# Optimization experiments

Hardware: AMD Instinct MI355X
Metric: run time of the kernel (lower is better)

Reference implementation:

```python
import jax, jax.numpy as jnp
import numpy as np

EPS = 1e-8  # torch F.cosine_similarity default eps


def setup_inputs() -> dict:
    key = jax.random.key(0)
    k1, k2 = jax.random.split(key)
    x = jax.random.normal(k1, (16384, 1024), dtype=jnp.float32)
    label = jax.random.randint(k2, (16384, 64), 0, 2).astype(jnp.int64)
    w = jnp.asarray(10.0, dtype=jnp.float32)  # nn.Parameter init_w
    b = jnp.asarray(-5.0, dtype=jnp.float32)  # nn.Parameter init_b
    return {"x": x, "label": label, "w": w, "b": b}


def reference(x, label, w, b):
    # Append the 'no-label' column for rows whose label vector is all zero.
    extra = (label.sum(axis=1) == 0).astype(label.dtype)[:, None]
    lab = jnp.concatenate([label, extra], axis=1).astype(x.dtype)  # [B, C]

    counts = lab.sum(axis=0)                  # [C] positives per centroid
    active = counts > 0                       # torch drops empty columns; we mask them

    # Centroids: mean of x over rows carrying each label (scatter-mean as GEMM).
    anchor = (lab.T @ x) / jnp.maximum(counts, 1.0)[:, None]   # [C, D]

    # Cosine similarity between every sample and every centroid.
    xn = jnp.maximum(jnp.linalg.norm(x, axis=1), EPS)          # [B]
    an = jnp.maximum(jnp.linalg.norm(anchor, axis=1), EPS)     # [C]
    cos = (x @ anchor.T) / (xn[:, None] * an[None, :])          # [B, C]

    logits = cos * w + b
    # Removing empty columns from softmax == setting their logits to -inf.
    logits = jnp.where(active[None, :], logits, -jnp.inf)
    logp = jax.nn.log_softmax(logits, axis=1)                   # [B, C]

    # Row expansion in torch duplicates sample i once per positive label j;
    # the logits row only depends on i, so CE over expanded rows is a
    # pair-weighted mean of -logp[i, j] over positive (i, j) pairs.
    n_pairs = lab.sum()
    nloss = -jnp.sum(jnp.where(lab > 0, logp, 0.0)) / n_pairs
    return nloss
```

## Files before the change

kernel.cpp:

```cpp
#include <hip/hip_runtime.h>
#include <hip/hip_bf16.h>
#include <stdint.h>

#define NROWS 16384
#define NDIM  1024
#define NLAB  64
#define NC    65
#define CPAD  80

typedef float float4v __attribute__((ext_vector_type(4)));
typedef short short8  __attribute__((ext_vector_type(8)));

static constexpr size_t SCALE_B = 0;
static constexpr size_t ACTB_B  = 320;
static constexpr size_t WSUM_B  = 400;
static constexpr size_t CNTF_B  = 448;
static constexpr size_t CNTP_B  = 1024;
static constexpr size_t MASK_B  = 83968;
static constexpr size_t XN2_B   = 215040;
static constexpr size_t LFRAG_B = 280576;
static constexpr size_t BFRAG_B = 2902016;
static constexpr size_t XAF_B   = 3065856;
static constexpr size_t XCOL_B  = 36620288;
static constexpr size_t PART_B  = 70174720;
static constexpr size_t SLAB    = (size_t)CPAD * NDIM * 4;
static constexpr size_t ANCH_SZ = (size_t)CPAD * NDIM * 4;
static constexpr size_t NRM_SZ  = (size_t)CPAD * 4 * 4;

__device__ __forceinline__ unsigned short bf16u(float f) {
    __hip_bfloat16 h = __float2bfloat16(f);
    return __builtin_bit_cast(unsigned short, h);
}
__device__ __forceinline__ unsigned pk2(float a, float b) {
    return (unsigned)bf16u(a) | ((unsigned)bf16u(b) << 16);
}

__global__ __launch_bounds__(256) void k01_prep(const float* __restrict__ x,
                                                const int* __restrict__ label,
                                                unsigned short* __restrict__ xAfrag,
                                                unsigned short* __restrict__ xcol,
                                                float* __restrict__ xn2g,
                                                unsigned long long* __restrict__ masks,
                                                unsigned* __restrict__ cntpart,
                                                unsigned short* __restrict__ lfrag) {
    __shared__ unsigned short xt[16][1040];
    __shared__ unsigned cnt[NC];
    __shared__ unsigned long long smask[64];
    int t = threadIdx.x;
    if (blockIdx.x < 1024) {
        int rt = blockIdx.x;
        int r = t >> 4, cpos = t & 15;
        const float4* src = (const float4*)(x + ((size_t)rt * 16 + r) * NDIM) + cpos;
        float4 f[16];
#pragma unroll
        for (int i = 0; i < 16; ++i) f[i] = src[i * 16];
        float sq = 0.f;
#pragma unroll
        for (int i = 0; i < 16; ++i) {
            sq += f[i].x * f[i].x + f[i].y * f[i].y + f[i].z * f[i].z + f[i].w * f[i].w;
            *(uint2*)&xt[r][cpos * 4 + i * 64] = make_uint2(pk2(f[i].x, f[i].y), pk2(f[i].z, f[i].w));
        }
#pragma unroll
        for (int m = 1; m < 16; m <<= 1) sq += __shfl_xor(sq, m, 16);
        if (cpos == 0) xn2g[rt * 16 + r] = sq;
        __syncthreads();
        {
            int slot = t & 63, wv = t >> 6;
            int q = slot >> 4, col = slot & 15;
#pragma unroll
            for (int s = 0; s < 8; ++s) {
                int kb = s * 4 + wv;
                uint4 v = *(const uint4*)&xt[col][kb * 32 + q * 8];
                ((uint4*)xAfrag)[((size_t)rt * 32 + kb) * 64 + slot] = v;
            }
        }
        {
            int rh8 = (t & 1) * 8, dg = t >> 1;
            uint4 R[8];
#pragma unroll
            for (int j = 0; j < 8; ++j) R[j] = *(const uint4*)&xt[rh8 + j][dg * 8];
            uint4* dst = (uint4*)xcol + (size_t)rt * 2048 + t * 8;
#pragma unroll
            for (int p = 0; p < 4; ++p) {
                unsigned lo[4], hi[4];
#pragma unroll
                for (int jj = 0; jj < 4; ++jj) {
                    unsigned A0 = ((const unsigned*)&R[2 * jj])[p];
                    unsigned B0 = ((const unsigned*)&R[2 * jj + 1])[p];
                    lo[jj] = __builtin_amdgcn_perm(B0, A0, 0x05040100u);
                    hi[jj] = __builtin_amdgcn_perm(B0, A0, 0x07060302u);
                }
                dst[2 * p]     = make_uint4(lo[0], lo[1], lo[2], lo[3]);
                dst[2 * p + 1] = make_uint4(hi[0], hi[1], hi[2], hi[3]);
            }
        }
        return;
    }
    int bid = blockIdx.x - 1024;
    if (t < NC) cnt[t] = 0;
    __syncthreads();
    int wave = t >> 6, lane = t & 63;
    int rowblock = bid * 64;
    unsigned creg = 0, zreg = 0;
#pragma unroll 4
    for (int p = 0; p < 16; ++p) {
        int row = rowblock + p * 4 + wave;
        int v = label[row * NLAB + lane];
        unsigned long long m = __ballot(v != 0);
        creg += (unsigned)((m >> lane) & 1ull);
        if (lane == 0) {
            masks[row] = m;
            smask[p * 4 + wave] = m;
            zreg += (m == 0ull) ? 1u : 0u;
        }
    }
    atomicAdd(&cnt[lane], creg);
    if (lane == 0 && zreg) atomicAdd(&cnt[64], zreg);
    __syncthreads();
    if (t < 80) cntpart[bid * 80 + t] = (t < NC) ? cnt[t] : 0u;
    for (int pid = t; pid < 640; pid += 256) {
        int rt2l = pid / 320, rem = pid % 320;
        int ct = rem >> 6, ln = rem & 63;
        int q = ln >> 4, col = ln & 15;
        int c = ct * 16 + col;
        int rbase = rt2l * 32 + q * 8;
        unsigned pk[4];
#pragma unroll
        for (int jp = 0; jp < 4; ++jp) {
            unsigned long long m0 = smask[rbase + jp * 2], m1 = smask[rbase + jp * 2 + 1];
            unsigned b0, b1;
            if (c < 64)       { b0 = (unsigned)((m0 >> c) & 1ull); b1 = (unsigned)((m1 >> c) & 1ull); }
            else if (c == 64) { b0 = (m0 == 0ull); b1 = (m1 == 0ull); }
            else              { b0 = 0u; b1 = 0u; }
            pk[jp] = (b0 ? 0x3F80u : 0u) | (b1 ? 0x3F800000u : 0u);
        }
        uint4 w = make_uint4(pk[0], pk[1], pk[2], pk[3]);
        ((uint4*)lfrag)[((size_t)(bid * 2 + rt2l) * 5 + ct) * 64 + ln] = w;
    }
}

__global__ __launch_bounds__(256) void k2_sums(const unsigned short* __restrict__ xcol,
                                               const unsigned short* __restrict__ lfrag,
                                               float* __restrict__ partial,
                                               int kslices) {
    int t = threadIdx.x, wave = t >> 6, lane = t & 63;
    int q = lane >> 4, col = lane & 15;
    int dgroup = blockIdx.x & 15, ks = blockIdx.x >> 4;
    int nkb = (NROWS / kslices) >> 5;
    int kb0 = ks * nkb;
    int d = dgroup * 64 + wave * 16 + col;
    const uint4* B = (const uint4*)xcol;
    const uint4* A = (const uint4*)lfrag;
    size_t bidx0 = (size_t)((d >> 3) * 16 + (q & 1) * 8 + (d & 7));
    int qh = q >> 1;

    float4v acc[5];
#pragma unroll
    for (int ct = 0; ct < 5; ++ct) acc[ct] = (float4v){0.f, 0.f, 0.f, 0.f};

    uint4 b0 = B[(size_t)((kb0 + 0) * 2 + qh) * 2048 + bidx0];
    uint4 a0[5];
#pragma unroll
    for (int ct = 0; ct < 5; ++ct) a0[ct] = A[((size_t)(kb0 + 0) * 5 + ct) * 64 + lane];
    uint4 b1 = B[(size_t)((kb0 + 1) * 2 + qh) * 2048 + bidx0];
    uint4 a1[5];
#pragma unroll
    for (int ct = 0; ct < 5; ++ct) a1[ct] = A[((size_t)(kb0 + 1) * 5 + ct) * 64 + lane];

    for (int i = 0; i < nkb; i += 2) {
        int p2 = i + 2 < nkb ? kb0 + i + 2 : kb0 + i;
        int p3 = i + 3 < nkb ? kb0 + i + 3 : kb0 + i + 1;
        {
            short8 bf = __builtin_bit_cast(short8, b0);
#pragma unroll
            for (int ct = 0; ct < 5; ++ct) {
                short8 af = __builtin_bit_cast(short8, a0[ct]);
                acc[ct] = __builtin_amdgcn_mfma_f32_16x16x32_bf16(af, bf, acc[ct], 0, 0, 0);
            }
            b0 = B[(size_t)(p2 * 2 + qh) * 2048 + bidx0];
#pragma unroll
            for (int ct = 0; ct < 5; ++ct) a0[ct] = A[((size_t)p2 * 5 + ct) * 64 + lane];
        }
        {
            short8 bf = __builtin_bit_cast(short8, b1);
#pragma unroll
            for (int ct = 0; ct < 5; ++ct) {
                short8 af = __builtin_bit_cast(short8, a1[ct]);
                acc[ct] = __builtin_amdgcn_mfma_f32_16x16x32_bf16(af, bf, acc[ct], 0, 0, 0);
            }
            b1 = B[(size_t)(p3 * 2 + qh) * 2048 + bidx0];
#pragma unroll
            for (int ct = 0; ct < 5; ++ct) a1[ct] = A[((size_t)p3 * 5 + ct) * 64 + lane];
        }
    }
    float* pb = partial + (size_t)ks * CPAD * NDIM;
#pragma unroll
    for (int ct = 0; ct < 5; ++ct)
#pragma unroll
        for (int reg = 0; reg < 4; ++reg)
            pb[(size_t)(ct * 16 + q * 4 + reg) * NDIM + d] = acc[ct][reg];
}

__global__ __launch_bounds__(256) void k2bA(const float* __restrict__ partial,
                                            int kslices,
                                            float* __restrict__ anchor_raw,
                                            float* __restrict__ norm2part) {
    __shared__ float red[4];
    int c = blockIdx.x >> 2, dq = blockIdx.x & 3, t = threadIdx.x;
    int d = dq * 256 + t;
    const float* p = partial + (size_t)c * NDIM + d;
    float s = 0.f;
#pragma unroll 8
    for (int sl = 0; sl < kslices; ++sl) s += p[(size_t)sl * CPAD * NDIM];
    anchor_raw[(size_t)c * NDIM + d] = s;
    float ss = s * s;
#pragma unroll
    for (int m = 32; m >= 1; m >>= 1) ss += __shfl_xor(ss, m, 64);
    if ((t & 63) == 0) red[t >> 6] = ss;
    __syncthreads();
    if (t == 0) norm2part[blockIdx.x] = red[0] + red[1] + red[2] + red[3];
}

__global__ __launch_bounds__(1024) void k2bB(const float* __restrict__ wptr,
                                             const unsigned* __restrict__ cntpart,
                                             const float* __restrict__ anchor_raw,
                                             const float* __restrict__ norm2part,
                                             unsigned short* __restrict__ bfrag,
                                             float* __restrict__ scale,
                                             unsigned char* __restrict__ actB,
                                             unsigned* __restrict__ countsF,
                                             float* __restrict__ wsum) {
    int c = blockIdx.x, t = threadIdx.x;
    __shared__ float red[16];
    __shared__ unsigned credu[4];
    __shared__ float bcast[1];
    if (c == 0 && t == 512) *wsum = 0.f;
    if (t < 256) {
        unsigned cv = cntpart[t * 80 + c];
#pragma unroll
        for (int m = 32; m >= 1; m >>= 1) cv += __shfl_xor(cv, m, 64);
        if ((t & 63) == 0) credu[t >> 6] = cv;
    }
    if (t == 0)
        bcast[0] = sqrtf(norm2part[c * 4] + norm2part[c * 4 + 1] +
                         norm2part[c * 4 + 2] + norm2part[c * 4 + 3]);
    __syncthreads();
    unsigned cnt = credu[0] + credu[1] + credu[2] + credu[3];
    float invc = 1.0f / (float)(cnt > 0u ? cnt : 1u);
    float a = anchor_raw[(size_t)c * NDIM + t] * invc;
    float an = fmaxf(bcast[0] * invc, 1e-8f);
    unsigned short h = bf16u(a / an);
    int ct = c >> 4, colc = c & 15;
    int kb = t >> 5, q = (t >> 3) & 3, j0 = t & 7;
    bfrag[((((size_t)ct * 32 + kb) * 64) + q * 16 + colc) * 8 + j0] = h;
    float hv = __bfloat162float(__builtin_bit_cast(__hip_bfloat16, h));
    float nb2 = hv * hv;
#pragma unroll
    for (int m = 32; m >= 1; m >>= 1) nb2 += __shfl_xor(nb2, m, 64);
    if ((t & 63) == 0) red[t >> 6] = nb2;
    __syncthreads();
    if (t == 0) {
        float n2 = 0.f;
#pragma unroll
        for (int j = 0; j < 16; ++j) n2 += red[j];
        scale[c] = (n2 > 0.f) ? (wptr[0] / sqrtf(n2)) : 0.f;
        actB[c] = (cnt > 0u) ? 1 : 0;
        countsF[c] = cnt;
    }
}

__global__ __launch_bounds__(256) void k3_loss(const unsigned short* __restrict__ xAfrag,
                                               const unsigned short* __restrict__ bfrag,
                                               const float* __restrict__ xn2g,
                                               const unsigned long long* __restrict__ masks,
                                               const unsigned char* __restrict__ actB,
                                               const float* __restrict__ scale,
                                               const float* __restrict__ bptr,
                                               float* __restrict__ wsum) {
    __shared__ float redsm[3][64][21];
    int t = threadIdx.x, wave = t >> 6, lane = t & 63;
    int q = lane >> 4, col = lane & 15;
    int rt = blockIdx.x;
    int rowbase = rt * 16;
    const uint4* A = (const uint4*)xAfrag + (size_t)rt * 32 * 64 + lane;
    const uint4* Bp = (const uint4*)bfrag + lane;
    int kb0 = wave * 8;

    float4v acc[5];
#pragma unroll
    for (int ct = 0; ct < 5; ++ct) acc[ct] = (float4v){0.f, 0.f, 0.f, 0.f};

    uint4 a0 = A[(size_t)(kb0 + 0) * 64], a1 = A[(size_t)(kb0 + 1) * 64];
    uint4 b0[5], b1[5];
#pragma unroll
    for (int ct = 0; ct < 5; ++ct) b0[ct] = Bp[(size_t)(ct * 32 + kb0 + 0) * 64];
#pragma unroll
    for (int ct = 0; ct < 5; ++ct) b1[ct] = Bp[(size_t)(ct * 32 + kb0 + 1) * 64];

    for (int s = 0; s < 8; s += 2) {
        int p2 = s + 2 < 8 ? kb0 + s + 2 : kb0 + s;
        int p3 = s + 3 < 8 ? kb0 + s + 3 : kb0 + s + 1;
        {
            short8 af = __builtin_bit_cast(short8, a0);
#pragma unroll
            for (int ct = 0; ct < 5; ++ct) {
                short8 bf = __builtin_bit_cast(short8, b0[ct]);
                acc[ct] = __builtin_amdgcn_mfma_f32_16x16x32_bf16(af, bf, acc[ct], 0, 0, 0);
            }
            a0 = A[(size_t)p2 * 64];
#pragma unroll
            for (int ct = 0; ct < 5; ++ct) b0[ct] = Bp[(size_t)(ct * 32 + p2) * 64];
        }
        {
            short8 af = __builtin_bit_cast(short8, a1);
#pragma unroll
            for (int ct = 0; ct < 5; ++ct) {
                short8 bf = __builtin_bit_cast(short8, b1[ct]);
                acc[ct] = __builtin_amdgcn_mfma_f32_16x16x32_bf16(af, bf, acc[ct], 0, 0, 0);
            }
            a1 = A[(size_t)p3 * 64];
#pragma unroll
            for (int ct = 0; ct < 5; ++ct) b1[ct] = Bp[(size_t)(ct * 32 + p3) * 64];
        }
    }

    if (wave) {
#pragma unroll
        for (int ct = 0; ct < 5; ++ct)
#pragma unroll
            for (int reg = 0; reg < 4; ++reg)
                redsm[wave - 1][lane][ct * 4 + reg] = acc[ct][reg];
    }
    __syncthreads();
    if (wave != 0) return;
#pragma unroll
    for (int w = 0; w < 3; ++w)
#pragma unroll
        for (int ct = 0; ct < 5; ++ct)
#pragma unroll
            for (int reg = 0; reg < 4; ++reg)
                acc[ct][reg] += redsm[w][lane][ct * 4 + reg];

    float bv = bptr[0];
    float sc[5]; unsigned char ab[5];
#pragma unroll
    for (int ct = 0; ct < 5; ++ct) { sc[ct] = scale[ct * 16 + col]; ab[ct] = actB[ct * 16 + col]; }

    float contrib = 0.f;
#pragma unroll
    for (int reg = 0; reg < 4; ++reg) {
        int rl = q * 4 + reg;
        int row = rowbase + rl;
        float inv = 1.0f / fmaxf(sqrtf(xn2g[row]), 1e-8f);
        unsigned long long mask = masks[row];
        float v[5]; float lmax = -1e30f;
#pragma unroll
        for (int ct = 0; ct < 5; ++ct) {
            float lg = acc[ct][reg] * sc[ct] * inv + bv;
            v[ct] = ab[ct] ? lg : -1e30f;
            lmax = fmaxf(lmax, v[ct]);
        }
#pragma unroll
        for (int m = 1; m < 16; m <<= 1) lmax = fmaxf(lmax, __shfl_xor(lmax, m, 16));
        float es = 0.f;
#pragma unroll
        for (int ct = 0; ct < 5; ++ct) es += expf(v[ct] - lmax);
#pragma unroll
        for (int m = 1; m < 16; m <<= 1) es += __shfl_xor(es, m, 16);
        float lse = lmax + logf(es);
        float ps = 0.f;
#pragma unroll
        for (int ct = 0; ct < 5; ++ct) {
            int c = ct * 16 + col;
            bool pos = (c < 64) ? (((mask >> c) & 1ull) != 0ull)
                                : ((c == 64) ? (mask == 0ull) : false);
            ps += pos ? v[ct] : 0.f;
        }
#pragma unroll
        for (int m = 1; m < 16; m <<= 1) ps += __shfl_xor(ps, m, 16);
        float npos = mask ? (float)__popcll(mask) : 1.0f;
        float crow = ps - npos * lse;
        if (col == 0) contrib += crow;
    }
#pragma unroll
    for (int m = 1; m < 64; m <<= 1) contrib += __shfl_xor(contrib, m, 64);
    if (lane == 0) atomicAdd(wsum, contrib);
}

__global__ void k4_final(const unsigned* __restrict__ countsF,
                         const float* __restrict__ wsum,
                         float* __restrict__ out) {
    if (threadIdx.x == 0 && blockIdx.x == 0) {
        float np = 0.f;
        for (int c = 0; c < NC; ++c) np += (float)countsF[c];
        out[0] = -wsum[0] / np;
    }
}

extern "C" void kernel_launch(void* const* d_in, const int* in_sizes, int n_in,
                              void* d_out, int out_size, void* d_ws, size_t ws_size,
                              hipStream_t stream) {
    (void)in_sizes; (void)n_in; (void)out_size;
    const float* x = (const float*)d_in[0];
    const int* label = (const int*)d_in[1];
    const float* w = (const float*)d_in[2];
    const float* b = (const float*)d_in[3];

    char* ws = (char*)d_ws;
    float* scale = (float*)(ws + SCALE_B);
    unsigned char* actB = (unsigned char*)(ws + ACTB_B);
    float* wsum = (float*)(ws + WSUM_B);
    unsigned* countsF = (unsigned*)(ws + CNTF_B);
    unsigned* cntpart = (unsigned*)(ws + CNTP_B);
    unsigned long long* masks = (unsigned long long*)(ws + MASK_B);
    float* xn2g = (float*)(ws + XN2_B);
    unsigned short* lfrag = (unsigned short*)(ws + LFRAG_B);
    unsigned short* bfrag = (unsigned short*)(ws + BFRAG_B);
    unsigned short* xAfrag = (unsigned short*)(ws + XAF_B);
    unsigned short* xcol = (unsigned short*)(ws + XCOL_B);
    float* partial = (float*)(ws + PART_B);

    int kslices = 64;
    while (kslices > 8 && PART_B + (size_t)kslices * SLAB + ANCH_SZ + NRM_SZ > ws_size)
        kslices >>= 1;
    float* anchor_raw = (float*)(ws + PART_B + (size_t)kslices * SLAB);
    float* norm2part = anchor_raw + CPAD * NDIM;

    hipLaunchKernelGGL(k01_prep, dim3(1024 + 256), dim3(256), 0, stream,
                       x, label, xAfrag, xcol, xn2g, masks, cntpart, lfrag);
    hipLaunchKernelGGL(k2_sums, dim3(16 * kslices), dim3(256), 0, stream,
                       xcol, lfrag, partial, kslices);
    hipLaunchKernelGGL(k2bA, dim3(CPAD * 4), dim3(256), 0, stream,
                       partial, kslices, anchor_raw, norm2part);
    hipLaunchKernelGGL(k2bB, dim3(CPAD), dim3(1024), 0, stream,
                       w, cntpart, anchor_raw, norm2part, bfrag, scale, actB, countsF, wsum);
    hipLaunchKernelGGL(k3_loss, dim3(NROWS / 16), dim3(256), 0, stream,
                       xAfrag, bfrag, xn2g, masks, actB, scale, b, wsum);
    hipLaunchKernelGGL(k4_final, dim3(1), dim3(64), 0, stream, countsF, wsum, (float*)d_out);
}
```

Measured before the change: 172.2 us.

## Drop transposed bf16 x copy; centroid GEMM reads fp32 x directly

The prep kernel no longer builds a transposed bf16 copy of x (xcol) through shared memory. It writes the MFMA A-fragments straight from global loads and reduces the row norms with shuffles plus a small shared array. The centroid-sum kernel now loads fp32 x column-strided from global memory and packs it to bf16 in registers before each MFMA. This removes a 32 MB write and its later read, but k2_sums now fetches twice the bytes per element with strided 4-byte loads and does extra conversion work in its inner loop.

```diff
diff --git a/kernel.cpp b/kernel.cpp
--- a/kernel.cpp
+++ b/kernel.cpp
@@ -21,7 +21,6 @@
 static constexpr size_t LFRAG_B = 280576;
 static constexpr size_t BFRAG_B = 2902016;
 static constexpr size_t XAF_B   = 3065856;
-static constexpr size_t XCOL_B  = 36620288;
 static constexpr size_t PART_B  = 70174720;
 static constexpr size_t SLAB    = (size_t)CPAD * NDIM * 4;
 static constexpr size_t ANCH_SZ = (size_t)CPAD * NDIM * 4;
@@ -35,65 +34,40 @@
     return (unsigned)bf16u(a) | ((unsigned)bf16u(b) << 16);
 }
 
-__global__ __launch_bounds__(256) void k01_prep(const float* __restrict__ x,
-                                                const int* __restrict__ label,
-                                                unsigned short* __restrict__ xAfrag,
-                                                unsigned short* __restrict__ xcol,
-                                                float* __restrict__ xn2g,
-                                                unsigned long long* __restrict__ masks,
-                                                unsigned* __restrict__ cntpart,
-                                                unsigned short* __restrict__ lfrag) {
-    __shared__ unsigned short xt[16][1040];
+__global__ __launch_bounds__(256, 4) void k01_prep(const float* __restrict__ x,
+                                                   const int* __restrict__ label,
+                                                   unsigned short* __restrict__ xAfrag,
+                                                   float* __restrict__ xn2g,
+                                                   unsigned long long* __restrict__ masks,
+                                                   unsigned* __restrict__ cntpart,
+                                                   unsigned short* __restrict__ lfrag) {
     __shared__ unsigned cnt[NC];
     __shared__ unsigned long long smask[64];
+    __shared__ float red[4][16];
     int t = threadIdx.x;
     if (blockIdx.x < 1024) {
         int rt = blockIdx.x;
-        int r = t >> 4, cpos = t & 15;
-        const float4* src = (const float4*)(x + ((size_t)rt * 16 + r) * NDIM) + cpos;
-        float4 f[16];
-#pragma unroll
-        for (int i = 0; i < 16; ++i) f[i] = src[i * 16];
+        int w = t >> 6, lane = t & 63, q = lane >> 4, col = lane & 15;
+        const float* rowp = x + ((size_t)rt * 16 + col) * NDIM;
+        uint4* dst = (uint4*)xAfrag + ((size_t)rt * 32 + w * 8) * 64 + lane;
         float sq = 0.f;
 #pragma unroll
-        for (int i = 0; i < 16; ++i) {
-            sq += f[i].x * f[i].x + f[i].y * f[i].y + f[i].z * f[i].z + f[i].w * f[i].w;
-            *(uint2*)&xt[r][cpos * 4 + i * 64] = make_uint2(pk2(f[i].x, f[i].y), pk2(f[i].z, f[i].w));
-        }
-#pragma unroll
-        for (int m = 1; m < 16; m <<= 1) sq += __shfl_xor(sq, m, 16);
-        if (cpos == 0) xn2g[rt * 16 + r] = sq;
+        for (int kb = 0; kb < 8; ++kb) {
+            int d0 = w * 256 + kb * 32 + q * 8;
+            float4 fa = *(const float4*)(rowp + d0);
+            float4 fb = *(const float4*)(rowp + d0 + 4);
+            sq += fa.x * fa.x + fa.y * fa.y + fa.z * fa.z + fa.w * fa.w
+                + fb.x * fb.x + fb.y * fb.y + fb.z * fb.z + fb.w * fb.w;
+            uint4 v;
+            v.x = pk2(fa.x, fa.y); v.y = pk2(fa.z, fa.w);
+            v.z = pk2(fb.x, fb.y); v.w = pk2(fb.z, fb.w);
+            dst[kb * 64] = v;
+        }
+        sq += __shfl_xor(sq, 16, 64);
+        sq += __shfl_xor(sq, 32, 64);
+        if (q == 0) red[w][col] = sq;
         __syncthreads();
-        {
-            int slot = t & 63, wv = t >> 6;
-            int q = slot >> 4, col = slot & 15;
-#pragma unroll
-            for (int s = 0; s < 8; ++s) {
-                int kb = s * 4 + wv;
-                uint4 v = *(const uint4*)&xt[col][kb * 32 + q * 8];
-                ((uint4*)xAfrag)[((size_t)rt * 32 + kb) * 64 + slot] = v;
-            }
-        }
-        {
-            int rh8 = (t & 1) * 8, dg = t >> 1;
-            uint4 R[8];
-#pragma unroll
-            for (int j = 0; j < 8; ++j) R[j] = *(const uint4*)&xt[rh8 + j][dg * 8];
-            uint4* dst = (uint4*)xcol + (size_t)rt * 2048 + t * 8;
-#pragma unroll
-            for (int p = 0; p < 4; ++p) {
-                unsigned lo[4], hi[4];
-#pragma unroll
-                for (int jj = 0; jj < 4; ++jj) {
-                    unsigned A0 = ((const unsigned*)&R[2 * jj])[p];
-                    unsigned B0 = ((const unsigned*)&R[2 * jj + 1])[p];
-                    lo[jj] = __builtin_amdgcn_perm(B0, A0, 0x05040100u);
-                    hi[jj] = __builtin_amdgcn_perm(B0, A0, 0x07060302u);
-                }
-                dst[2 * p]     = make_uint4(lo[0], lo[1], lo[2], lo[3]);
-                dst[2 * p + 1] = make_uint4(hi[0], hi[1], hi[2], hi[3]);
-            }
-        }
+        if (t < 16) xn2g[rt * 16 + t] = red[0][t] + red[1][t] + red[2][t] + red[3][t];
         return;
     }
     int bid = blockIdx.x - 1024;
@@ -139,7 +113,7 @@
     }
 }
 
-__global__ __launch_bounds__(256) void k2_sums(const unsigned short* __restrict__ xcol,
+__global__ __launch_bounds__(256) void k2_sums(const float* __restrict__ x,
                                                const unsigned short* __restrict__ lfrag,
                                                float* __restrict__ partial,
                                                int kslices) {
@@ -149,46 +123,60 @@
     int nkb = (NROWS / kslices) >> 5;
     int kb0 = ks * nkb;
     int d = dgroup * 64 + wave * 16 + col;
-    const uint4* B = (const uint4*)xcol;
     const uint4* A = (const uint4*)lfrag;
-    size_t bidx0 = (size_t)((d >> 3) * 16 + (q & 1) * 8 + (d & 7));
-    int qh = q >> 1;
+    const float* xb = x + d;
 
     float4v acc[5];
 #pragma unroll
     for (int ct = 0; ct < 5; ++ct) acc[ct] = (float4v){0.f, 0.f, 0.f, 0.f};
 
-    uint4 b0 = B[(size_t)((kb0 + 0) * 2 + qh) * 2048 + bidx0];
-    uint4 a0[5];
-#pragma unroll
-    for (int ct = 0; ct < 5; ++ct) a0[ct] = A[((size_t)(kb0 + 0) * 5 + ct) * 64 + lane];
-    uint4 b1 = B[(size_t)((kb0 + 1) * 2 + qh) * 2048 + bidx0];
-    uint4 a1[5];
-#pragma unroll
-    for (int ct = 0; ct < 5; ++ct) a1[ct] = A[((size_t)(kb0 + 1) * 5 + ct) * 64 + lane];
+    float f0[8], f1[8];
+    uint4 a0[5], a1[5];
+    {
+        const float* p = xb + (size_t)(kb0 * 32 + q * 8) * NDIM;
+#pragma unroll
+        for (int j = 0; j < 8; ++j) f0[j] = p[(size_t)j * NDIM];
+#pragma unroll
+        for (int ct = 0; ct < 5; ++ct) a0[ct] = A[((size_t)kb0 * 5 + ct) * 64 + lane];
+        const float* p1 = xb + (size_t)((kb0 + 1) * 32 + q * 8) * NDIM;
+#pragma unroll
+        for (int j = 0; j < 8; ++j) f1[j] = p1[(size_t)j * NDIM];
+#pragma unroll
+        for (int ct = 0; ct < 5; ++ct) a1[ct] = A[((size_t)(kb0 + 1) * 5 + ct) * 64 + lane];
+    }
 
     for (int i = 0; i < nkb; i += 2) {
         int p2 = i + 2 < nkb ? kb0 + i + 2 : kb0 + i;
         int p3 = i + 3 < nkb ? kb0 + i + 3 : kb0 + i + 1;
         {
-            short8 bf = __builtin_bit_cast(short8, b0);
+            uint4 bq;
+            bq.x = pk2(f0[0], f0[1]); bq.y = pk2(f0[2], f0[3]);
+            bq.z = pk2(f0[4], f0[5]); bq.w = pk2(f0[6], f0[7]);
+            short8 bf = __builtin_bit_cast(short8, bq);
 #pragma unroll
             for (int ct = 0; ct < 5; ++ct) {
                 short8 af = __builtin_bit_cast(short8, a0[ct]);
                 acc[ct] = __builtin_amdgcn_mfma_f32_16x16x32_bf16(af, bf, acc[ct], 0, 0, 0);
             }
-            b0 = B[(size_t)(p2 * 2 + qh) * 2048 + bidx0];
+            const float* p = xb + (size_t)(p2 * 32 + q * 8) * NDIM;
+#pragma unroll
+            for (int j = 0; j < 8; ++j) f0[j] = p[(size_t)j * NDIM];
 #pragma unroll
             for (int ct = 0; ct < 5; ++ct) a0[ct] = A[((size_t)p2 * 5 + ct) * 64 + lane];
         }
         {
-            short8 bf = __builtin_bit_cast(short8, b1);
+            uint4 bq;
+            bq.x = pk2(f1[0], f1[1]); bq.y = pk2(f1[2], f1[3]);
+            bq.z = pk2(f1[4], f1[5]); bq.w = pk2(f1[6], f1[7]);
+            short8 bf = __builtin_bit_cast(short8, bq);
 #pragma unroll
             for (int ct = 0; ct < 5; ++ct) {
                 short8 af = __builtin_bit_cast(short8, a1[ct]);
                 acc[ct] = __builtin_amdgcn_mfma_f32_16x16x32_bf16(af, bf, acc[ct], 0, 0, 0);
             }
-            b1 = B[(size_t)(p3 * 2 + qh) * 2048 + bidx0];
+            const float* p = xb + (size_t)(p3 * 32 + q * 8) * NDIM;
+#pragma unroll
+            for (int j = 0; j < 8; ++j) f1[j] = p[(size_t)j * NDIM];
 #pragma unroll
             for (int ct = 0; ct < 5; ++ct) a1[ct] = A[((size_t)p3 * 5 + ct) * 64 + lane];
         }
@@ -417,7 +405,6 @@
     unsigned short* lfrag = (unsigned short*)(ws + LFRAG_B);
     unsigned short* bfrag = (unsigned short*)(ws + BFRAG_B);
     unsigned short* xAfrag = (unsigned short*)(ws + XAF_B);
-    unsigned short* xcol = (unsigned short*)(ws + XCOL_B);
     float* partial = (float*)(ws + PART_B);
 
     int kslices = 64;
@@ -427,9 +414,9 @@
     float* norm2part = anchor_raw + CPAD * NDIM;
 
     hipLaunchKernelGGL(k01_prep, dim3(1024 + 256), dim3(256), 0, stream,
-                       x, label, xAfrag, xcol, xn2g, masks, cntpart, lfrag);
+                       x, label, xAfrag, xn2g, masks, cntpart, lfrag);
     hipLaunchKernelGGL(k2_sums, dim3(16 * kslices), dim3(256), 0, stream,
-                       xcol, lfrag, partial, kslices);
+                       x, lfrag, partial, kslices);
     hipLaunchKernelGGL(k2bA, dim3(CPAD * 4), dim3(256), 0, stream,
                        partial, kslices, anchor_raw, norm2part);
     hipLaunchKernelGGL(k2bB, dim3(CPAD), dim3(1024), 0, stream,
```

Result: faster. 168.5 us (-2.1%).
